# Kernel tuning notes

Measured on AMD Instinct MI355X. Metric: run time of the kernel, lower is better.

Reference implementation:

```python
import jax, jax.numpy as jnp
import numpy as np

DIM = 768
NUM_HEADS = 12
HEAD_DIM = DIM // NUM_HEADS
EPS = 1e-5


def setup_inputs() -> dict:
    key = jax.random.key(0)
    ks = jax.random.split(key, 9)
    s = 1.0 / np.sqrt(DIM)
    x = jax.random.normal(ks[0], (8, 1024, DIM), dtype=jnp.float32)
    Wq = jax.random.uniform(ks[1], (DIM, DIM), jnp.float32, -s, s)
    bq = jax.random.uniform(ks[2], (DIM,), jnp.float32, -s, s)
    Wk = jax.random.uniform(ks[3], (DIM, DIM), jnp.float32, -s, s)
    bk = jax.random.uniform(ks[4], (DIM,), jnp.float32, -s, s)
    Wv = jax.random.uniform(ks[5], (DIM, DIM), jnp.float32, -s, s)
    bv = jax.random.uniform(ks[6], (DIM,), jnp.float32, -s, s)
    Wo = jax.random.uniform(ks[7], (DIM, DIM), jnp.float32, -s, s)
    bo = jax.random.uniform(ks[8], (DIM,), jnp.float32, -s, s)
    ln_g = jnp.ones((DIM,), jnp.float32)
    ln_b = jnp.zeros((DIM,), jnp.float32)
    return {"x": x, "Wq": Wq, "bq": bq, "Wk": Wk, "bk": bk, "Wv": Wv,
            "bv": bv, "Wo": Wo, "bo": bo, "ln_g": ln_g, "ln_b": ln_b}


def _layernorm(h, g, b):
    mu = jnp.mean(h, axis=-1, keepdims=True)
    var = jnp.mean(jnp.square(h - mu), axis=-1, keepdims=True)
    return (h - mu) * jax.lax.rsqrt(var + EPS) * g + b


def reference(x, Wq, bq, Wk, bk, Wv, bv, Wo, bo, ln_g, ln_b):
    B, N, C = x.shape
    H, D = NUM_HEADS, HEAD_DIM
    scaling = D ** -0.5
    q = (x @ Wq.T + bq) * scaling          # [B,N,C]
    k = x @ Wk.T + bk
    v = x @ Wv.T + bv
    q = q.reshape(B, N, H, D).transpose(0, 2, 1, 3)  # [B,H,N,D]
    k = k.reshape(B, N, H, D).transpose(0, 2, 1, 3)
    v = v.reshape(B, N, H, D).transpose(0, 2, 1, 3)
    scores = jnp.einsum('bhnd,bhmd->bhnm', q, k)     # [B,H,N,N]
    probs = jax.nn.softmax(scores.astype(jnp.float32), axis=-1).astype(scores.dtype)
    attn = jnp.einsum('bhnm,bhmd->bhnd', probs, v)   # [B,H,N,D]
    attn = attn.transpose(0, 2, 1, 3).reshape(B, N, C)
    attn = _layernorm(attn, ln_g, ln_b)
    return attn @ Wo.T + bo
```

## Files before the change

### kernel.cpp

```cpp
#include <hip/hip_runtime.h>
#include <hip/hip_bf16.h>
#include <stdint.h>


using short8  = __attribute__((ext_vector_type(8))) short;
using short4v = __attribute__((ext_vector_type(4))) short;
using floatx4 = __attribute__((ext_vector_type(4))) float;

#define LOG2E 1.44269504088896340736f

typedef __attribute__((address_space(3))) uint32_t lds_u32;
typedef const __attribute__((address_space(1))) uint32_t glb_u32;
__device__ __forceinline__ void async_copy16(const void* g, void* l) {
  __builtin_amdgcn_global_load_lds((glb_u32*)g, (lds_u32*)l, 16, 0, 0);
}

__device__ __forceinline__ float b2f(int s) {
  return __builtin_bit_cast(float, (uint32_t)((uint16_t)s) << 16);
}
__device__ __forceinline__ short f2b(float f) {
  uint32_t u = __builtin_bit_cast(uint32_t, f);
  u += 0x7fffu + ((u >> 16) & 1u);
  return (short)(u >> 16);
}
__device__ __forceinline__ uint32_t pk2(float a, float b) {
#if defined(__has_builtin) && __has_builtin(__builtin_amdgcn_cvt_pk_bf16_f32)
  typedef __bf16 bf16x2 __attribute__((ext_vector_type(2)));
  return __builtin_bit_cast(uint32_t, __builtin_amdgcn_cvt_pk_bf16_f32(a, b));
#else
  return (uint32_t)(uint16_t)f2b(a) | ((uint32_t)(uint16_t)f2b(b) << 16);
#endif
}
__device__ __forceinline__ floatx4 mfma16x16(short4v a, short4v b, floatx4 c) {
#if defined(__has_builtin) && __has_builtin(__builtin_amdgcn_mfma_f32_16x16x16bf16_1k)
  return __builtin_amdgcn_mfma_f32_16x16x16bf16_1k(a, b, c, 0, 0, 0);
#else
  floatx4 d = c;
  asm volatile("v_mfma_f32_16x16x16_bf16 %0, %1, %2, %0"
               : "+v"(d) : "v"(a), "v"(b));
  return d;
#endif
}
__device__ __forceinline__ float loadf(const void* p, int idx, bool f32) {
  return f32 ? ((const float*)p)[idx] : b2f(((const short*)p)[idx]);
}
__device__ __forceinline__ short8 load8f(const void* p, int idx) {
  const float* q = (const float*)p + idx;
  float4 x0 = *(const float4*)q, x1 = *(const float4*)(q + 4);
  short8 v = {f2b(x0.x), f2b(x0.y), f2b(x0.z), f2b(x0.w),
              f2b(x1.x), f2b(x1.y), f2b(x1.z), f2b(x1.w)};
  return v;
}

__global__ __launch_bounds__(256) void cvt1_k(
    const void* __restrict__ x, const void* __restrict__ wq,
    const void* __restrict__ wk, const void* __restrict__ wv,
    const void* __restrict__ bq, const void* __restrict__ bk,
    const void* __restrict__ bv, short* __restrict__ xb,
    short* __restrict__ wqkvb, short* __restrict__ bqkvb,
    const unsigned short* __restrict__ probe) {
  if (probe[0] == 0x3F80u) return;
  int idx = blockIdx.x * 256 + threadIdx.x;
  if (idx < 786432) { *(short8*)&xb[idx * 8] = load8f(x, idx * 8); return; }
  idx -= 786432;
  if (idx < 73728) { *(short8*)&wqkvb[idx * 8] = load8f(wq, idx * 8); return; }
  idx -= 73728;
  if (idx < 73728) { *(short8*)&wqkvb[589824 + idx * 8] = load8f(wk, idx * 8); return; }
  idx -= 73728;
  if (idx < 73728) { *(short8*)&wqkvb[1179648 + idx * 8] = load8f(wv, idx * 8); return; }
  idx -= 73728;
  if (idx < 96) { *(short8*)&bqkvb[idx * 8] = load8f(bq, idx * 8); return; }
  idx -= 96;
  if (idx < 96) { *(short8*)&bqkvb[768 + idx * 8] = load8f(bk, idx * 8); return; }
  idx -= 96;
  if (idx < 96) { *(short8*)&bqkvb[1536 + idx * 8] = load8f(bv, idx * 8); return; }
}

__global__ __launch_bounds__(256) void cvt2_k(const void* __restrict__ wo,
                                              const void* __restrict__ bo,
                                              short* __restrict__ wob,
                                              short* __restrict__ bob,
                                              const unsigned short* __restrict__ probe) {
  if (probe[0] == 0x3F80u) return;
  int idx = blockIdx.x * 256 + threadIdx.x;
  if (idx < 73728) { *(short8*)&wob[idx * 8] = load8f(wo, idx * 8); return; }
  idx -= 73728;
  if (idx < 96) { *(short8*)&bob[idx * 8] = load8f(bo, idx * 8); return; }
}

__device__ __forceinline__ void gemm_core(const short* __restrict__ Ab,
                                          const short* __restrict__ Bb,
                                          short* sA, short* sB,
                                          floatx4 (&acc)[4][4]) {
  const int t = threadIdx.x;
  const int w = t >> 6, l = t & 63;
  const int lrow = l & 15, quad = l >> 4;
  const int rw = (w >> 1) * 64, cw = (w & 1) * 64;
  for (int k0 = 0; k0 < 768; k0 += 32) {
#pragma unroll
    for (int i = 0; i < 2; i++) {
      const int ci = i * 256 + t;
      const int row = ci >> 2, ch = ci & 3;
      async_copy16(Ab + row * 768 + k0 + ch * 8, (char*)sA + ci * 16);
      async_copy16(Bb + row * 768 + k0 + ch * 8, (char*)sB + ci * 16);
    }
    __syncthreads();
    short8 af[4], bf[4];
#pragma unroll
    for (int i = 0; i < 4; i++)
      af[i] = *(const short8*)&sA[(rw + i * 16 + lrow) * 32 + quad * 8];
#pragma unroll
    for (int j = 0; j < 4; j++)
      bf[j] = *(const short8*)&sB[(cw + j * 16 + lrow) * 32 + quad * 8];
#pragma unroll
    for (int i = 0; i < 4; i++)
#pragma unroll
      for (int j = 0; j < 4; j++)
        acc[i][j] =
            __builtin_amdgcn_mfma_f32_16x16x32_bf16(af[i], bf[j], acc[i][j], 0, 0, 0);
    __syncthreads();
  }
}

__global__ __launch_bounds__(256) void gemm_qkv_k(
    const void* __restrict__ x, const short* __restrict__ xb,
    const void* __restrict__ Wq, const void* __restrict__ Wk,
    const void* __restrict__ Wv, const short* __restrict__ wqkvb,
    const void* __restrict__ bq, const void* __restrict__ bk,
    const void* __restrict__ bv, const short* __restrict__ bqkvb,
    short* __restrict__ qo, short* __restrict__ ko, short* __restrict__ vo,
    const unsigned short* __restrict__ probe) {
  __shared__ __align__(16) short sA[4096];
  __shared__ __align__(16) short sB[4096];
  const bool f32 = (probe[0] != 0x3F80u);
  const int atile = blockIdx.x, btile = blockIdx.y;
  const int sel = btile / 6;

  const short* Ab = (f32 ? xb : (const short*)x) + atile * 98304;
  const short* Bb;
  const short* biasb;
  if (f32) {
    Bb = wqkvb + btile * 98304;
    biasb = bqkvb + sel * 768;
  } else {
    const void* Wsel = sel == 0 ? Wq : (sel == 1 ? Wk : Wv);
    Bb = (const short*)Wsel + (btile - sel * 6) * 98304;
    biasb = (const short*)(sel == 0 ? bq : (sel == 1 ? bk : bv));
  }

  floatx4 acc[4][4] = {};
  gemm_core(Ab, Bb, sA, sB, acc);

  const int t = threadIdx.x, w = t >> 6, l = t & 63;
  const int lrow = l & 15, quad = l >> 4;
  const int rw = (w >> 1) * 64, cw = (w & 1) * 64;
  const int nbase = (btile - sel * 6) * 128;
#pragma unroll
  for (int i = 0; i < 4; i++) {
    const int ra0 = atile * 128 + rw + i * 16 + quad * 4;
    const int bidx = ra0 >> 10, n_in_b = ra0 & 1023;
#pragma unroll
    for (int j = 0; j < 4; j++) {
      const int cb = nbase + cw + j * 16 + lrow;
      const float bias = b2f(biasb[cb]);
      const int hh = cb >> 6, dd = cb & 63;
      if (sel == 2) {
        short4v pv;
#pragma unroll
        for (int r = 0; r < 4; r++) pv[r] = f2b(acc[i][j][r] + bias);
        *(short4v*)&vo[(bidx * 12 + hh) * 65536 + dd * 1024 + n_in_b] = pv;
      } else {
        const int base = (bidx * 12 + hh) * 65536 + dd;
        short* dst = sel == 0 ? qo : ko;
#pragma unroll
        for (int r = 0; r < 4; r++) {
          float v = acc[i][j][r] + bias;
          if (sel == 0) v *= (0.125f * LOG2E);
          dst[base + (n_in_b + r) * 64] = f2b(v);
        }
      }
    }
  }
}

__global__ __launch_bounds__(256) void gemm_out_k(
    const short* __restrict__ ln, const void* __restrict__ Wo,
    const short* __restrict__ wob, const void* __restrict__ bo,
    const short* __restrict__ bob, void* __restrict__ out,
    const unsigned short* __restrict__ probe) {
  __shared__ __align__(16) short sA[4096];
  __shared__ __align__(16) short sB[4096];
  const bool f32 = (probe[0] != 0x3F80u);
  const int atile = blockIdx.x, btile = blockIdx.y;
  const short* Ab = ln + atile * 98304;
  const short* Bb = (f32 ? wob : (const short*)Wo) + btile * 98304;
  const short* biasb = f32 ? bob : (const short*)bo;

  floatx4 acc[4][4] = {};
  gemm_core(Ab, Bb, sA, sB, acc);

  const int t = threadIdx.x, w = t >> 6, l = t & 63;
  const int lrow = l & 15, quad = l >> 4;
  const int rw = (w >> 1) * 64, cw = (w & 1) * 64;
#pragma unroll
  for (int i = 0; i < 4; i++) {
    const int ra0 = atile * 128 + rw + i * 16 + quad * 4;
#pragma unroll
    for (int j = 0; j < 4; j++) {
      const int cb = btile * 128 + cw + j * 16 + lrow;
      const float bias = b2f(biasb[cb]);
#pragma unroll
      for (int r = 0; r < 4; r++) {
        float v = acc[i][j][r] + bias;
        if (f32) ((float*)out)[(ra0 + r) * 768 + cb] = v;
        else     ((short*)out)[(ra0 + r) * 768 + cb] = f2b(v);
      }
    }
  }
}

__global__ __launch_bounds__(256, 3) void attn_k(const short* __restrict__ q,
                                                 const short* __restrict__ k,
                                                 const short* __restrict__ vt,
                                                 short* __restrict__ o) {
  __shared__ __align__(16) short sQ[8192];
  __shared__ __align__(16) short sK[2][4096];
  __shared__ __align__(16) short sV[2][4096];

  const int t = threadIdx.x, w = t >> 6, l = t & 63;
  const int lrow = l & 15, quad = l >> 4;
  const int qt = blockIdx.x, bh = blockIdx.y;
  const int b = bh / 12, h = bh % 12;
  const short* qb = q + bh * 65536 + qt * 8192;
  const short* kb = k + bh * 65536;
  const short* vb = vt + bh * 65536;

#pragma unroll
  for (int i = 0; i < 4; i++) {
    const int ci = i * 256 + t;
    const int row = ci >> 3, sc = ci & 7, gc = sc ^ (row & 7);
    async_copy16(qb + row * 64 + gc * 8, (char*)sQ + ci * 16);
  }
#pragma unroll
  for (int i = 0; i < 2; i++) {
    const int ci = i * 256 + t;
    const int row = ci >> 3, sc = ci & 7, gc = sc ^ (row & 7);
    async_copy16(kb + row * 64 + gc * 8, (char*)sK[0] + ci * 16);
    async_copy16(vb + row * 1024 + gc * 8, (char*)sV[0] + ci * 16);
  }
  __syncthreads();

  short8 qf[2][2];
#pragma unroll
  for (int qh = 0; qh < 2; qh++) {
    const int qr = w * 32 + qh * 16 + lrow;
#pragma unroll
    for (int dc = 0; dc < 2; dc++)
      qf[qh][dc] = *(const short8*)&sQ[qr * 64 + ((dc * 4 + quad) ^ (qr & 7)) * 8];
  }

  float l_run[2] = {0.f, 0.f};
  floatx4 o_acc[2][4] = {};

  for (int it = 0; it < 16; it++) {
    const int cur = it & 1;
    if (it < 15) {
      const int kv0 = (it + 1) * 64, nxt = cur ^ 1;
#pragma unroll
      for (int i = 0; i < 2; i++) {
        const int ci = i * 256 + t;
        const int row = ci >> 3, sc = ci & 7, gc = sc ^ (row & 7);
        async_copy16(kb + (kv0 + row) * 64 + gc * 8, (char*)sK[nxt] + ci * 16);
        async_copy16(vb + row * 1024 + kv0 + gc * 8, (char*)sV[nxt] + ci * 16);
      }
    }

    short4v pf[2][4];
#pragma unroll
    for (int j = 0; j < 4; j++) {
      const int kr = j * 16 + lrow;
      short8 kf0 = *(const short8*)&sK[cur][kr * 64 + (quad ^ (kr & 7)) * 8];
      short8 kf1 = *(const short8*)&sK[cur][kr * 64 + ((4 + quad) ^ (kr & 7)) * 8];
#pragma unroll
      for (int qh = 0; qh < 2; qh++) {
        floatx4 st = {};
        st = __builtin_amdgcn_mfma_f32_16x16x32_bf16(kf0, qf[qh][0], st, 0, 0, 0);
        st = __builtin_amdgcn_mfma_f32_16x16x32_bf16(kf1, qf[qh][1], st, 0, 0, 0);
        const float p0 = exp2f(st[0]), p1 = exp2f(st[1]);
        const float p2 = exp2f(st[2]), p3 = exp2f(st[3]);
        l_run[qh] += (p0 + p1) + (p2 + p3);
        uint2 pp = {pk2(p0, p1), pk2(p2, p3)};
        pf[qh][j] = __builtin_bit_cast(short4v, pp);
      }
    }

#pragma unroll
    for (int j2 = 0; j2 < 4; j2++) {
      const int vd = j2 * 16 + lrow;
#pragma unroll
      for (int tt = 0; tt < 4; tt++) {
        const int c8 = (tt * 2 + (quad >> 1)) ^ (vd & 7);
        short4v vf = *(const short4v*)&sV[cur][vd * 64 + c8 * 8 + (quad & 1) * 4];
        o_acc[0][j2] = mfma16x16(pf[0][tt], vf, o_acc[0][j2]);
        o_acc[1][j2] = mfma16x16(pf[1][tt], vf, o_acc[1][j2]);
      }
    }
    __syncthreads();
  }

#pragma unroll
  for (int qh = 0; qh < 2; qh++) {
    l_run[qh] += __shfl_xor(l_run[qh], 16);
    l_run[qh] += __shfl_xor(l_run[qh], 32);
  }
#pragma unroll
  for (int qh = 0; qh < 2; qh++) {
    float inv_l[4];
#pragma unroll
    for (int r = 0; r < 4; r++) inv_l[r] = 1.0f / __shfl(l_run[qh], quad * 4 + r);
    const int n0 = qt * 128 + w * 32 + qh * 16 + quad * 4;
#pragma unroll
    for (int j2 = 0; j2 < 4; j2++) {
      const int d = j2 * 16 + lrow;
#pragma unroll
      for (int r = 0; r < 4; r++)
        o[(b * 1024 + n0 + r) * 768 + h * 64 + d] = f2b(o_acc[qh][j2][r] * inv_l[r]);
    }
  }
}

__global__ __launch_bounds__(256) void ln_k(const short* __restrict__ in,
                                            const void* __restrict__ g,
                                            const void* __restrict__ be,
                                            short* __restrict__ out,
                                            const unsigned short* __restrict__ probe) {
  const bool f32 = (probe[0] != 0x3F80u);
  const int w = threadIdx.x >> 6, l = threadIdx.x & 63;
  const int row = blockIdx.x * 4 + w;
  const short* rp = in + row * 768;
  float v[12];
  float s = 0.f, ss = 0.f;
#pragma unroll
  for (int c = 0; c < 3; c++) {
    ushort4 u = *(const ushort4*)&rp[(c * 64 + l) * 4];
    float f0 = b2f(u.x), f1 = b2f(u.y), f2 = b2f(u.z), f3 = b2f(u.w);
    v[c * 4 + 0] = f0; v[c * 4 + 1] = f1; v[c * 4 + 2] = f2; v[c * 4 + 3] = f3;
    s += (f0 + f1) + (f2 + f3);
    ss += (f0 * f0 + f1 * f1) + (f2 * f2 + f3 * f3);
  }
#pragma unroll
  for (int msk = 1; msk < 64; msk <<= 1) {
    s += __shfl_xor(s, msk);
    ss += __shfl_xor(ss, msk);
  }
  const float mu = s * (1.f / 768.f);
  const float rstd = rsqrtf(ss * (1.f / 768.f) - mu * mu + 1e-5f);
  short* op = out + row * 768;
#pragma unroll
  for (int c = 0; c < 3; c++) {
    const int base = (c * 64 + l) * 4;
    ushort4 r;
    r.x = (unsigned short)(unsigned)f2b((v[c * 4 + 0] - mu) * rstd * loadf(g, base + 0, f32) + loadf(be, base + 0, f32));
    r.y = (unsigned short)(unsigned)f2b((v[c * 4 + 1] - mu) * rstd * loadf(g, base + 1, f32) + loadf(be, base + 1, f32));
    r.z = (unsigned short)(unsigned)f2b((v[c * 4 + 2] - mu) * rstd * loadf(g, base + 2, f32) + loadf(be, base + 2, f32));
    r.w = (unsigned short)(unsigned)f2b((v[c * 4 + 3] - mu) * rstd * loadf(g, base + 3, f32) + loadf(be, base + 3, f32));
    *(ushort4*)&op[base] = r;
  }
}

extern "C" void kernel_launch(void* const* d_in, const int* in_sizes, int n_in,
                              void* d_out, int out_size, void* d_ws, size_t ws_size,
                              hipStream_t stream) {
  const void* x    = d_in[0];
  const void* Wq   = d_in[1];
  const void* bq   = d_in[2];
  const void* Wk   = d_in[3];
  const void* bk   = d_in[4];
  const void* Wv   = d_in[5];
  const void* bv   = d_in[6];
  const void* Wo   = d_in[7];
  const void* bo   = d_in[8];
  const void* ln_g = d_in[9];
  const void* ln_b = d_in[10];
  const unsigned short* probe = (const unsigned short*)d_in[9];

  char* ws = (char*)d_ws;
  const size_t SZ = 12582912;
  if (ws_size < 3 * SZ) return;
  short* qbuf = (short*)ws;
  short* kbuf = (short*)(ws + SZ);
  short* vtb  = (short*)(ws + 2 * SZ);

  char* outc = (char*)d_out;
  short* wqkvb = (short*)outc;
  short* bqkvb = (short*)(outc + 3538944);
  short* xb    = (short*)(outc + 12582912);
  short* wob   = (short*)(ws + SZ);
  short* bob   = (short*)(ws + SZ + 1179648);

  dim3 blk(256);
  cvt1_k<<<3938, blk, 0, stream>>>(x, Wq, Wk, Wv, bq, bk, bv, xb, wqkvb, bqkvb, probe);
  gemm_qkv_k<<<dim3(64, 18), blk, 0, stream>>>(x, xb, Wq, Wk, Wv, wqkvb, bq, bk, bv,
                                               bqkvb, qbuf, kbuf, vtb, probe);
  attn_k<<<dim3(8, 96), blk, 0, stream>>>(qbuf, kbuf, vtb, (short*)d_out);
  cvt2_k<<<289, blk, 0, stream>>>(Wo, bo, wob, bob, probe);
  ln_k<<<2048, blk, 0, stream>>>((short*)d_out, ln_g, ln_b, qbuf, probe);
  gemm_out_k<<<dim3(64, 6), blk, 0, stream>>>(qbuf, Wo, wob, bo, bob, d_out, probe);
}
```

Baseline: 254.4 us.

## Fuse Wo conversion into layernorm, compute softmax row sums via MFMA, swap attention grid

Three changes. The separate Wo/bo bf16 conversion kernel is folded into the layernorm launch as extra blocks, which removes one kernel launch. The softmax denominators are now accumulated with an MFMA against a ones vector instead of scalar adds plus cross-lane shuffles, moving VALU work onto the matrix units. The attention grid is transposed so that blocks sharing the same head are no longer adjacent in launch order, which changes L2 locality for K/V reuse. The row sum now comes from the bf16-rounded probabilities, which slightly alters numerics.

```diff
diff --git a/kernel.cpp b/kernel.cpp
--- a/kernel.cpp
+++ b/kernel.cpp
@@ -76,18 +76,6 @@
   if (idx < 96) { *(short8*)&bqkvb[1536 + idx * 8] = load8f(bv, idx * 8); return; }
 }
 
-__global__ __launch_bounds__(256) void cvt2_k(const void* __restrict__ wo,
-                                              const void* __restrict__ bo,
-                                              short* __restrict__ wob,
-                                              short* __restrict__ bob,
-                                              const unsigned short* __restrict__ probe) {
-  if (probe[0] == 0x3F80u) return;
-  int idx = blockIdx.x * 256 + threadIdx.x;
-  if (idx < 73728) { *(short8*)&wob[idx * 8] = load8f(wo, idx * 8); return; }
-  idx -= 73728;
-  if (idx < 96) { *(short8*)&bob[idx * 8] = load8f(bo, idx * 8); return; }
-}
-
 __device__ __forceinline__ void gemm_core(const short* __restrict__ Ab,
                                           const short* __restrict__ Bb,
                                           short* sA, short* sB,
@@ -229,7 +217,7 @@
 
   const int t = threadIdx.x, w = t >> 6, l = t & 63;
   const int lrow = l & 15, quad = l >> 4;
-  const int qt = blockIdx.x, bh = blockIdx.y;
+  const int bh = blockIdx.x, qt = blockIdx.y;
   const int b = bh / 12, h = bh % 12;
   const short* qb = q + bh * 65536 + qt * 8192;
   const short* kb = k + bh * 65536;
@@ -259,7 +247,9 @@
       qf[qh][dc] = *(const short8*)&sQ[qr * 64 + ((dc * 4 + quad) ^ (qr & 7)) * 8];
   }
 
-  float l_run[2] = {0.f, 0.f};
+  const short one_b = (short)0x3F80;
+  const short4v ones4 = {one_b, one_b, one_b, one_b};
+  floatx4 l_acc[2] = {};
   floatx4 o_acc[2][4] = {};
 
   for (int it = 0; it < 16; it++) {
@@ -288,10 +278,15 @@
         st = __builtin_amdgcn_mfma_f32_16x16x32_bf16(kf1, qf[qh][1], st, 0, 0, 0);
         const float p0 = exp2f(st[0]), p1 = exp2f(st[1]);
         const float p2 = exp2f(st[2]), p3 = exp2f(st[3]);
-        l_run[qh] += (p0 + p1) + (p2 + p3);
         uint2 pp = {pk2(p0, p1), pk2(p2, p3)};
         pf[qh][j] = __builtin_bit_cast(short4v, pp);
       }
+    }
+
+#pragma unroll
+    for (int tt = 0; tt < 4; tt++) {
+      l_acc[0] = mfma16x16(pf[0][tt], ones4, l_acc[0]);
+      l_acc[1] = mfma16x16(pf[1][tt], ones4, l_acc[1]);
     }
 
 #pragma unroll
@@ -310,14 +305,9 @@
 
 #pragma unroll
   for (int qh = 0; qh < 2; qh++) {
-    l_run[qh] += __shfl_xor(l_run[qh], 16);
-    l_run[qh] += __shfl_xor(l_run[qh], 32);
-  }
-#pragma unroll
-  for (int qh = 0; qh < 2; qh++) {
     float inv_l[4];
 #pragma unroll
-    for (int r = 0; r < 4; r++) inv_l[r] = 1.0f / __shfl(l_run[qh], quad * 4 + r);
+    for (int r = 0; r < 4; r++) inv_l[r] = 1.0f / l_acc[qh][r];
     const int n0 = qt * 128 + w * 32 + qh * 16 + quad * 4;
 #pragma unroll
     for (int j2 = 0; j2 < 4; j2++) {
@@ -329,12 +319,24 @@
   }
 }
 
-__global__ __launch_bounds__(256) void ln_k(const short* __restrict__ in,
-                                            const void* __restrict__ g,
-                                            const void* __restrict__ be,
-                                            short* __restrict__ out,
-                                            const unsigned short* __restrict__ probe) {
+__global__ __launch_bounds__(256) void lncvt_k(const short* __restrict__ in,
+                                               const void* __restrict__ g,
+                                               const void* __restrict__ be,
+                                               short* __restrict__ out,
+                                               const void* __restrict__ wo,
+                                               const void* __restrict__ bo,
+                                               short* __restrict__ wob,
+                                               short* __restrict__ bob,
+                                               const unsigned short* __restrict__ probe) {
   const bool f32 = (probe[0] != 0x3F80u);
+  if (blockIdx.x >= 2048) {
+    if (!f32) return;
+    int idx = (blockIdx.x - 2048) * 256 + threadIdx.x;
+    if (idx < 73728) { *(short8*)&wob[idx * 8] = load8f(wo, idx * 8); return; }
+    idx -= 73728;
+    if (idx < 96) { *(short8*)&bob[idx * 8] = load8f(bo, idx * 8); }
+    return;
+  }
   const int w = threadIdx.x >> 6, l = threadIdx.x & 63;
   const int row = blockIdx.x * 4 + w;
   const short* rp = in + row * 768;
@@ -402,8 +404,8 @@
   cvt1_k<<<3938, blk, 0, stream>>>(x, Wq, Wk, Wv, bq, bk, bv, xb, wqkvb, bqkvb, probe);
   gemm_qkv_k<<<dim3(64, 18), blk, 0, stream>>>(x, xb, Wq, Wk, Wv, wqkvb, bq, bk, bv,
                                                bqkvb, qbuf, kbuf, vtb, probe);
-  attn_k<<<dim3(8, 96), blk, 0, stream>>>(qbuf, kbuf, vtb, (short*)d_out);
-  cvt2_k<<<289, blk, 0, stream>>>(Wo, bo, wob, bob, probe);
-  ln_k<<<2048, blk, 0, stream>>>((short*)d_out, ln_g, ln_b, qbuf, probe);
+  attn_k<<<dim3(96, 8), blk, 0, stream>>>(qbuf, kbuf, vtb, (short*)d_out);
+  lncvt_k<<<2337, blk, 0, stream>>>((short*)d_out, ln_g, ln_b, qbuf,
+                                    Wo, bo, wob, bob, probe);
   gemm_out_k<<<dim3(64, 6), blk, 0, stream>>>(qbuf, Wo, wob, bo, bob, d_out, probe);
 }
```

After: 246.1 us. 3.3% less time.
